# Kernel tuning notes

Measured on AMD Instinct MI355X. Metric: run time of the kernel, lower is better.

## Reference

```python
import jax, jax.numpy as jnp
import numpy as np

L_SPAN = 8          # max event span length
MAX_ITER = 3        # args.max_iteration + 1
RATE = 0.3          # confidence threshold for edge creation
BETA_INTRA = 0.7
BETA_INTER = 0.3


def setup_inputs() -> dict:
    key = jax.random.key(0)
    ks = jax.random.split(key, 16)
    n_sents, S, D = 64, 512, 768
    E, P, NL, H, C = 2000, 20000, 128, 512, 3
    sc = lambda fan: 1.0 / np.sqrt(fan)
    return {
        'sent_emb': jax.random.normal(ks[0], (n_sents, S, D), jnp.float32),
        'W_proj': jax.random.normal(ks[1], (D, NL), jnp.float32) * sc(D),
        'W1': jax.random.normal(ks[2], (2 * D + NL, H), jnp.float32) * sc(2 * D + NL),
        'b1': jnp.zeros((H,), jnp.float32),
        'W2': jax.random.normal(ks[3], (H, C), jnp.float32) * sc(H),
        'b2': jnp.zeros((C,), jnp.float32),
        'W_self': jax.random.normal(ks[4], (NL, NL), jnp.float32) * sc(NL),
        'W_intra': jax.random.normal(ks[5], (NL, NL), jnp.float32) * sc(NL),
        'W_inter': jax.random.normal(ks[6], (NL, NL), jnp.float32) * sc(NL),
        'event_sent': jax.random.randint(ks[7], (E,), 0, n_sents, jnp.int32),
        'event_start': jax.random.randint(ks[8], (E,), 0, S - L_SPAN, jnp.int32),
        'event_len': jax.random.randint(ks[9], (E,), 0, L_SPAN, jnp.int32),
        'pair1': jax.random.randint(ks[10], (P,), 0, E, jnp.int32),
        'pair2': jax.random.randint(ks[11], (P,), 0, E, jnp.int32),
        'rel_type': jax.random.randint(ks[12], (P,), 0, 2, jnp.int32),
        'target': jax.random.randint(ks[13], (P,), 0, 3, jnp.int32),
    }


def _extract_events(sent_emb, event_sent, event_start, event_len):
    # ragged span mean: spans have length 1..L_SPAN
    S = sent_emb.shape[1]
    lens = (event_len + 1).astype(sent_emb.dtype)            # [E]
    offs = jnp.arange(L_SPAN)
    idx = jnp.clip(event_start[:, None] + offs[None, :], 0, S - 1)  # [E, L]
    tok = sent_emb[event_sent[:, None], idx]                 # [E, L, D] gather
    mask = (offs[None, :] < (event_len + 1)[:, None]).astype(sent_emb.dtype)
    return (tok * mask[:, :, None]).sum(1) / lens[:, None]   # [E, D]


def reference(sent_emb, W_proj, W1, b1, W2, b2, W_self, W_intra, W_inter,
              event_sent, event_start, event_len, pair1, pair2, rel_type, target):
    E = event_sent.shape[0]
    e_emb = _extract_events(sent_emb, event_sent, event_start, event_len)   # [E, 768]
    event_pair_embed = jnp.concatenate([e_emb[pair1], e_emb[pair2]], axis=-1)  # [P, 1536]
    x = e_emb @ W_proj                                                      # [E, n_last]

    seg = jax.ops.segment_sum
    loss = jnp.float32(0.0)
    logits = None
    for it in range(MAX_ITER):
        diff = x[pair1] - x[pair2]                                          # [P, n_last]
        feats = jnp.concatenate([event_pair_embed, diff], axis=-1)          # [P, 1536+n_last]
        logits = jax.nn.relu(feats @ W1 + b1) @ W2 + b2                     # [P, C]
        logp = jax.nn.log_softmax(logits, axis=-1)
        ce = -jnp.take_along_axis(logp, target[:, None], axis=-1).mean()
        loss = loss + ce / (it + 1)

        # dynamic graph construction from predictions
        p = jax.nn.softmax(logits, axis=-1)
        conf = p.max(-1) > RATE
        argm = p.argmax(-1)
        f = lambda m: jax.lax.stop_gradient(m.astype(x.dtype))[:, None]
        mi1 = f(conf & (argm == 1) & (rel_type == 0))   # intra: pair1 -> pair2
        mi2 = f(conf & (argm == 2) & (rel_type == 0))   # intra reversed
        me1 = f(conf & (argm == 1) & (rel_type == 1))   # inter
        me2 = f(conf & (argm == 2) & (rel_type == 1))

        # intra aggregation (includes self-loop)
        s_intra = seg(x[pair1] * mi1, pair2, num_segments=E) + \
                  seg(x[pair2] * mi2, pair1, num_segments=E) + x
        c_intra = seg(mi1[:, 0], pair2, num_segments=E) + \
                  seg(mi2[:, 0], pair1, num_segments=E) + 1.0
        agg_intra = s_intra / c_intra[:, None]

        s_inter = seg(x[pair1] * me1, pair2, num_segments=E) + \
                  seg(x[pair2] * me2, pair1, num_segments=E)
        c_inter = seg(me1[:, 0], pair2, num_segments=E) + \
                  seg(me2[:, 0], pair1, num_segments=E)
        agg_inter = s_inter / jnp.maximum(c_inter, 1.0)[:, None]

        x = jax.nn.relu(x @ W_self + BETA_INTRA * (agg_intra @ W_intra)
                        + BETA_INTER * (agg_inter @ W_inter))
    return loss, logits
```

## Files before the change

kernel.cpp:

```cpp
#include <hip/hip_runtime.h>
#include <hip/hip_bf16.h>


#define D_DIM 768
#define H_DIM 512
#define NL_DIM 128

#define FTM 128
#define FTN 64
#define FKB 32
#define FKZ 4

__global__ __launch_bounds__(256) void gemm_fused(
    const float* __restrict__ Ag, const float* __restrict__ W1,
    const float* __restrict__ W_proj,
    float* __restrict__ A1, float* __restrict__ A2, float* __restrict__ X0, int M)
{
    __shared__ float As[2][FKB][FTM + 4];
    __shared__ float Bs[2][FKB][FTN];
    int t = threadIdx.x;
    int bx = blockIdx.x;
    int m0 = blockIdx.y * FTM;
    int kbase = blockIdx.z * (D_DIM / FKZ);
    const float* Bt; float* Ct; int ldb, ldc;
    if (bx < 8)       { Bt = W1 + bx * 64;                           ldb = 512; Ct = A1 + bx * 64;        ldc = 512; }
    else if (bx < 16) { Bt = W1 + (size_t)768 * 512 + (bx - 8) * 64; ldb = 512; Ct = A2 + (bx - 8) * 64;  ldc = 512; }
    else              { Bt = W_proj + (bx - 16) * 64;                ldb = 128; Ct = X0 + (bx - 16) * 64; ldc = 128; }

    int ar  = t >> 3;
    int ac4 = (t & 7) * 4;
    int br  = t >> 4;
    int bc4 = (t & 15) * 4;
    int tm  = t >> 4;
    int tn  = t & 15;

    float acc[8][4] = {};
    const int NT = (D_DIM / FKZ) / FKB;
    float4 pa[4], pb[2];

#pragma unroll
    for (int p = 0; p < 4; ++p) {
        int row = m0 + ar + 32 * p;
        pa[p] = (row < M) ? *(const float4*)(Ag + (size_t)row * D_DIM + kbase + ac4)
                          : make_float4(0.f, 0.f, 0.f, 0.f);
    }
#pragma unroll
    for (int p = 0; p < 2; ++p)
        pb[p] = *(const float4*)(Bt + (size_t)(kbase + br + 16 * p) * ldb + bc4);
#pragma unroll
    for (int p = 0; p < 4; ++p) {
        As[0][ac4 + 0][ar + 32 * p] = pa[p].x;
        As[0][ac4 + 1][ar + 32 * p] = pa[p].y;
        As[0][ac4 + 2][ar + 32 * p] = pa[p].z;
        As[0][ac4 + 3][ar + 32 * p] = pa[p].w;
    }
#pragma unroll
    for (int p = 0; p < 2; ++p)
        *(float4*)&Bs[0][br + 16 * p][bc4] = pb[p];
    __syncthreads();

    for (int kt = 0; kt < NT; ++kt) {
        int b = kt & 1;
        if (kt + 1 < NT) {
            int k0 = kbase + (kt + 1) * FKB;
#pragma unroll
            for (int p = 0; p < 4; ++p) {
                int row = m0 + ar + 32 * p;
                pa[p] = (row < M) ? *(const float4*)(Ag + (size_t)row * D_DIM + k0 + ac4)
                                  : make_float4(0.f, 0.f, 0.f, 0.f);
            }
#pragma unroll
            for (int p = 0; p < 2; ++p)
                pb[p] = *(const float4*)(Bt + (size_t)(k0 + br + 16 * p) * ldb + bc4);
        }
#pragma unroll
        for (int k = 0; k < FKB; ++k) {
            float4 a0 = *(const float4*)&As[b][k][tm * 4];
            float4 a1 = *(const float4*)&As[b][k][64 + tm * 4];
            float4 bv = *(const float4*)&Bs[b][k][tn * 4];
            acc[0][0] += a0.x * bv.x; acc[0][1] += a0.x * bv.y; acc[0][2] += a0.x * bv.z; acc[0][3] += a0.x * bv.w;
            acc[1][0] += a0.y * bv.x; acc[1][1] += a0.y * bv.y; acc[1][2] += a0.y * bv.z; acc[1][3] += a0.y * bv.w;
            acc[2][0] += a0.z * bv.x; acc[2][1] += a0.z * bv.y; acc[2][2] += a0.z * bv.z; acc[2][3] += a0.z * bv.w;
            acc[3][0] += a0.w * bv.x; acc[3][1] += a0.w * bv.y; acc[3][2] += a0.w * bv.z; acc[3][3] += a0.w * bv.w;
            acc[4][0] += a1.x * bv.x; acc[4][1] += a1.x * bv.y; acc[4][2] += a1.x * bv.z; acc[4][3] += a1.x * bv.w;
            acc[5][0] += a1.y * bv.x; acc[5][1] += a1.y * bv.y; acc[5][2] += a1.y * bv.z; acc[5][3] += a1.y * bv.w;
            acc[6][0] += a1.z * bv.x; acc[6][1] += a1.z * bv.y; acc[6][2] += a1.z * bv.z; acc[6][3] += a1.z * bv.w;
            acc[7][0] += a1.w * bv.x; acc[7][1] += a1.w * bv.y; acc[7][2] += a1.w * bv.z; acc[7][3] += a1.w * bv.w;
        }
        if (kt + 1 < NT) {
            int nb = (kt + 1) & 1;
#pragma unroll
            for (int p = 0; p < 4; ++p) {
                As[nb][ac4 + 0][ar + 32 * p] = pa[p].x;
                As[nb][ac4 + 1][ar + 32 * p] = pa[p].y;
                As[nb][ac4 + 2][ar + 32 * p] = pa[p].z;
                As[nb][ac4 + 3][ar + 32 * p] = pa[p].w;
            }
#pragma unroll
            for (int p = 0; p < 2; ++p)
                *(float4*)&Bs[nb][br + 16 * p][bc4] = pb[p];
        }
        __syncthreads();
    }
#pragma unroll
    for (int half = 0; half < 2; ++half) {
#pragma unroll
        for (int i = 0; i < 4; ++i) {
            int row = m0 + half * 64 + tm * 4 + i;
            if (row < M) {
                float* cp = Ct + (size_t)row * ldc + tn * 4;
                atomicAdd(&cp[0], acc[half * 4 + i][0]);
                atomicAdd(&cp[1], acc[half * 4 + i][1]);
                atomicAdd(&cp[2], acc[half * 4 + i][2]);
                atomicAdd(&cp[3], acc[half * 4 + i][3]);
            }
        }
    }
}

#define KB 32
#define TM 64
#define TN 64

struct Smem {
    float As[KB][TM + 4];
    float Bs[KB][TN];
};

__device__ __forceinline__ void tile_gemm(
    const float* __restrict__ A, int lda,
    const float* __restrict__ Bt, int ldb,
    int m0, int M, int K, Smem& sm, float acc[4][4], int t)
{
    int tm = t >> 4, tn = t & 15;
    for (int k0 = 0; k0 < K; k0 += KB) {
#pragma unroll
        for (int r = 0; r < 2; ++r) {
            int row = (t >> 3) + 32 * r;
            int c4 = (t & 7) * 4;
            float4 av = make_float4(0.f, 0.f, 0.f, 0.f);
            if (m0 + row < M)
                av = *(const float4*)(A + (size_t)(m0 + row) * lda + k0 + c4);
            sm.As[c4 + 0][row] = av.x;
            sm.As[c4 + 1][row] = av.y;
            sm.As[c4 + 2][row] = av.z;
            sm.As[c4 + 3][row] = av.w;
        }
#pragma unroll
        for (int r = 0; r < 2; ++r) {
            int row = (t >> 4) + 16 * r;
            int c4 = (t & 15) * 4;
            *(float4*)&sm.Bs[row][c4] =
                *(const float4*)(Bt + (size_t)(k0 + row) * ldb + c4);
        }
        __syncthreads();
#pragma unroll
        for (int k = 0; k < KB; ++k) {
            float4 a = *(const float4*)&sm.As[k][tm * 4];
            float4 b = *(const float4*)&sm.Bs[k][tn * 4];
            acc[0][0] += a.x * b.x; acc[0][1] += a.x * b.y; acc[0][2] += a.x * b.z; acc[0][3] += a.x * b.w;
            acc[1][0] += a.y * b.x; acc[1][1] += a.y * b.y; acc[1][2] += a.y * b.z; acc[1][3] += a.y * b.w;
            acc[2][0] += a.z * b.x; acc[2][1] += a.z * b.y; acc[2][2] += a.z * b.z; acc[2][3] += a.z * b.w;
            acc[3][0] += a.w * b.x; acc[3][1] += a.w * b.y; acc[3][2] += a.w * b.z; acc[3][3] += a.w * b.w;
        }
        __syncthreads();
    }
}

__global__ __launch_bounds__(256) void gemm_y_uv(
    const float* __restrict__ x, const float* __restrict__ W1k,
    const float* __restrict__ A1, const float* __restrict__ A2,
    const float* __restrict__ b1,
    float* __restrict__ U, float* __restrict__ V, int M)
{
    __shared__ Smem sm;
    int t = threadIdx.x;
    int n0 = blockIdx.x * TN;
    int m0 = blockIdx.y * TM;
    float acc[4][4] = {};
    tile_gemm(x, NL_DIM, W1k + n0, H_DIM, m0, M, NL_DIM, sm, acc, t);
    int tm = t >> 4, tn = t & 15;
    float4 b1v = *(const float4*)(b1 + n0 + tn * 4);
#pragma unroll
    for (int i = 0; i < 4; ++i) {
        int row = m0 + tm * 4 + i;
        if (row < M) {
            size_t off = (size_t)row * H_DIM + n0 + tn * 4;
            float4 a1v = *(const float4*)(A1 + off);
            float4 a2v = *(const float4*)(A2 + off);
            float4 u, v;
            u.x = acc[i][0] + a1v.x + b1v.x;  v.x = a2v.x - acc[i][0];
            u.y = acc[i][1] + a1v.y + b1v.y;  v.y = a2v.y - acc[i][1];
            u.z = acc[i][2] + a1v.z + b1v.z;  v.z = a2v.z - acc[i][2];
            u.w = acc[i][3] + a1v.w + b1v.w;  v.w = a2v.w - acc[i][3];
            *(float4*)(U + off) = u;
            *(float4*)(V + off) = v;
        }
    }
}

__global__ __launch_bounds__(256) void gemm_update3(
    const float* __restrict__ x, const float* __restrict__ aggI, const float* __restrict__ aggE,
    const float* __restrict__ Ws, const float* __restrict__ Wi, const float* __restrict__ We,
    float* __restrict__ xn, int M)
{
    __shared__ Smem sm;
    int t = threadIdx.x;
    int n0 = blockIdx.x * TN;
    int m0 = blockIdx.y * TM;
    float acc[4][4] = {};
    tile_gemm(x,    NL_DIM, Ws + n0, NL_DIM, m0, M, NL_DIM, sm, acc, t);
    tile_gemm(aggI, NL_DIM, Wi + n0, NL_DIM, m0, M, NL_DIM, sm, acc, t);
    tile_gemm(aggE, NL_DIM, We + n0, NL_DIM, m0, M, NL_DIM, sm, acc, t);
    int tm = t >> 4, tn = t & 15;
#pragma unroll
    for (int i = 0; i < 4; ++i) {
        int row = m0 + tm * 4 + i;
        if (row < M)
            *(float4*)(xn + (size_t)row * NL_DIM + n0 + tn * 4) =
                make_float4(fmaxf(acc[i][0], 0.f), fmaxf(acc[i][1], 0.f),
                            fmaxf(acc[i][2], 0.f), fmaxf(acc[i][3], 0.f));
    }
}

__global__ __launch_bounds__(192) void extract_kernel(
    const float* __restrict__ sent_emb, const int* __restrict__ es,
    const int* __restrict__ st, const int* __restrict__ el,
    float* __restrict__ e_emb)
{
    int e = blockIdx.x;
    int t = threadIdx.x;
    int s = es[e];
    int start = st[e];
    int len = el[e] + 1;
    const float* base = sent_emb + ((size_t)s * 512 + start) * D_DIM;
    float4 a = make_float4(0.f, 0.f, 0.f, 0.f);
    for (int k = 0; k < len; ++k) {
        float4 v = ((const float4*)(base + (size_t)k * D_DIM))[t];
        a.x += v.x; a.y += v.y; a.z += v.z; a.w += v.w;
    }
    float inv = 1.0f / (float)len;
    ((float4*)(e_emb + (size_t)e * D_DIM))[t] =
        make_float4(a.x * inv, a.y * inv, a.z * inv, a.w * inv);
}

__global__ __launch_bounds__(256) void zero4_kernel(float4* __restrict__ p, int n4)
{
    int i = blockIdx.x * 256 + threadIdx.x;
    if (i < n4) p[i] = make_float4(0.f, 0.f, 0.f, 0.f);
}

__global__ __launch_bounds__(256) void pair_kernel(
    const float* __restrict__ U, const float* __restrict__ V,
    const float* __restrict__ X, const float* __restrict__ W2,
    const float* __restrict__ b2,
    const int* __restrict__ pair1, const int* __restrict__ pair2,
    const int* __restrict__ rel, const int* __restrict__ tgt,
    float* s_intra, float* s_inter, float* c_intra, float* c_inter,
    float* __restrict__ ce_out, float* logits_out, int P, int do_scatter)
{
    __shared__ float ce_sh[4];
    int t = threadIdx.x;
    int wave = t >> 6;
    int lane = t & 63;
    int base = lane * 8;
    float w2f[24];
    {
        const float4* w2p = (const float4*)(W2 + (size_t)base * 3);
#pragma unroll
        for (int q = 0; q < 6; ++q) *(float4*)&w2f[q * 4] = w2p[q];
    }
    float b20 = b2[0], b21 = b2[1], b22 = b2[2];
    int p0 = (blockIdx.x * 4 + wave) * 4;

    int pi1[4], pi2[4];
#pragma unroll
    for (int q = 0; q < 4; ++q) {
        int p = min(p0 + q, P - 1);
        pi1[q] = pair1[p];
        pi2[q] = pair2[p];
    }
    float uf[4][8], vf[4][8];
#pragma unroll
    for (int q = 0; q < 4; ++q) {
        const float4* up = (const float4*)(U + (size_t)pi1[q] * H_DIM + base);
        const float4* vp = (const float4*)(V + (size_t)pi2[q] * H_DIM + base);
        *(float4*)&uf[q][0] = up[0]; *(float4*)&uf[q][4] = up[1];
        *(float4*)&vf[q][0] = vp[0]; *(float4*)&vf[q][4] = vp[1];
    }

    float ce = 0.f;
#pragma unroll
    for (int q = 0; q < 4; ++q) {
        int p = p0 + q;
        if (p >= P) break;
        float l0 = 0.f, l1 = 0.f, l2 = 0.f;
#pragma unroll
        for (int i = 0; i < 8; ++i) {
            float h = fmaxf(uf[q][i] + vf[q][i], 0.f);
            l0 += h * w2f[i * 3 + 0];
            l1 += h * w2f[i * 3 + 1];
            l2 += h * w2f[i * 3 + 2];
        }
#pragma unroll
        for (int off = 32; off > 0; off >>= 1) {
            l0 += __shfl_xor(l0, off);
            l1 += __shfl_xor(l1, off);
            l2 += __shfl_xor(l2, off);
        }
        l0 += b20; l1 += b21; l2 += b22;
        float m = fmaxf(l0, fmaxf(l1, l2));
        float lse = m + logf(expf(l0 - m) + expf(l1 - m) + expf(l2 - m));
        int tg = tgt[p];
        float lt = (tg == 0) ? l0 : ((tg == 1) ? l1 : l2);
        ce += lse - lt;
        if (logits_out && lane == 0) {
            logits_out[(size_t)p * 3 + 0] = l0;
            logits_out[(size_t)p * 3 + 1] = l1;
            logits_out[(size_t)p * 3 + 2] = l2;
        }
        if (do_scatter) {
            int argm = 0; float mx = l0;
            if (l1 > mx) { mx = l1; argm = 1; }
            if (l2 > mx) { mx = l2; argm = 2; }
            if (argm != 0) {
                int r = rel[p];
                int src = (argm == 1) ? pi1[q] : pi2[q];
                int dst = (argm == 1) ? pi2[q] : pi1[q];
                float* sacc = (r == 0) ? s_intra : s_inter;
                float* cacc = (r == 0) ? c_intra : c_inter;
                const float* xs = X + (size_t)src * NL_DIM;
                float* sd = sacc + (size_t)dst * NL_DIM;
                atomicAdd(&sd[lane], xs[lane]);
                atomicAdd(&sd[lane + 64], xs[lane + 64]);
                if (lane == 0) atomicAdd(&cacc[dst], 1.0f);
            }
        }
    }
    if (lane == 0) ce_sh[wave] = ce;
    __syncthreads();
    if (t == 0) ce_out[blockIdx.x] = ce_sh[0] + ce_sh[1] + ce_sh[2] + ce_sh[3];
}

__global__ __launch_bounds__(256) void agg_kernel(
    const float* __restrict__ s_intra, const float* __restrict__ s_inter,
    const float* __restrict__ c_intra, const float* __restrict__ c_inter,
    const float* __restrict__ X,
    float* __restrict__ aggI, float* __restrict__ aggE, int n)
{
    int i = blockIdx.x * 256 + threadIdx.x;
    if (i >= n) return;
    int e = i >> 7;
    float ci = c_intra[e] + 1.0f;
    float cf = fmaxf(c_inter[e], 1.0f);
    aggI[i] = 0.7f * (s_intra[i] + X[i]) / ci;
    aggE[i] = 0.3f * s_inter[i] / cf;
}

__global__ __launch_bounds__(256) void loss_kernel(
    const float* __restrict__ ce, int nblk, int P, float* __restrict__ out)
{
    int t = threadIdx.x;
    float acc = 0.f;
    for (int it = 0; it < 3; ++it) {
        float w = 1.0f / ((float)P * (float)(it + 1));
        for (int i = t; i < nblk; i += 256)
            acc += ce[(size_t)it * nblk + i] * w;
    }
    __shared__ float red[256];
    red[t] = acc;
    __syncthreads();
    for (int s = 128; s > 0; s >>= 1) {
        if (t < s) red[t] += red[t + s];
        __syncthreads();
    }
    if (t == 0) out[0] = red[0];
}

extern "C" void kernel_launch(void* const* d_in, const int* in_sizes, int n_in,
                              void* d_out, int out_size, void* d_ws, size_t ws_size,
                              hipStream_t stream)
{
    const float* sent_emb  = (const float*)d_in[0];
    const float* W_proj    = (const float*)d_in[1];
    const float* W1        = (const float*)d_in[2];
    const float* b1        = (const float*)d_in[3];
    const float* W2        = (const float*)d_in[4];
    const float* b2        = (const float*)d_in[5];
    const float* W_self    = (const float*)d_in[6];
    const float* W_intra   = (const float*)d_in[7];
    const float* W_inter   = (const float*)d_in[8];
    const int* event_sent  = (const int*)d_in[9];
    const int* event_start = (const int*)d_in[10];
    const int* event_len   = (const int*)d_in[11];
    const int* pair1       = (const int*)d_in[12];
    const int* pair2       = (const int*)d_in[13];
    const int* rel_type    = (const int*)d_in[14];
    const int* target      = (const int*)d_in[15];

    int E = in_sizes[9];
    int P = in_sizes[12];
    float* out = (float*)d_out;
    float* ws  = (float*)d_ws;

    size_t o = 0;
    float* e_emb   = ws + o; o += (size_t)E * D_DIM;
    float* A1      = ws + o; o += (size_t)E * H_DIM;
    float* A2      = ws + o; o += (size_t)E * H_DIM;
    float* X0      = ws + o; o += (size_t)E * NL_DIM;
    float* V       = ws + o; o += (size_t)E * H_DIM;
    float* X1      = ws + o; o += (size_t)E * NL_DIM;
    float* s_intra = ws + o; o += (size_t)E * NL_DIM;
    float* s_inter = ws + o; o += (size_t)E * NL_DIM;
    float* c_intra = ws + o; o += (size_t)E;
    float* c_inter = ws + o; o += (size_t)E;
    float* aggI    = ws + o; o += (size_t)E * NL_DIM;
    float* aggE    = ws + o; o += (size_t)E * NL_DIM;
    int NBLK = (P + 15) / 16;
    float* ceb     = ws + o; o += (size_t)3 * NBLK;
    float* U       = e_emb;

    int cz4 = E * (H_DIM * 2 + NL_DIM) / 4;
    zero4_kernel<<<(cz4 + 255) / 256, 256, 0, stream>>>((float4*)A1, cz4);
    extract_kernel<<<E, 192, 0, stream>>>(sent_emb, event_sent, event_start, event_len, e_emb);

    dim3 gF(18, (E + FTM - 1) / FTM, FKZ);
    gemm_fused<<<gF, 256, 0, stream>>>(e_emb, W1, W_proj, A1, A2, X0, E);

    const float* W1k = W1 + (size_t)2 * D_DIM * H_DIM;
    dim3 gY(H_DIM / TN, (E + TM - 1) / TM);
    dim3 gU(NL_DIM / TN, (E + TM - 1) / TM);
    float* xcur = X0;
    float* xnext = X1;
    int zn4 = (E * NL_DIM * 2 + E * 2) / 4;
    for (int it = 0; it < 3; ++it) {
        int last = (it == 2);
        gemm_y_uv<<<gY, 256, 0, stream>>>(xcur, W1k, A1, A2, b1, U, V, E);
        if (!last)
            zero4_kernel<<<(zn4 + 255) / 256, 256, 0, stream>>>((float4*)s_intra, zn4);
        pair_kernel<<<NBLK, 256, 0, stream>>>(U, V, xcur, W2, b2,
                                              pair1, pair2, rel_type, target,
                                              s_intra, s_inter, c_intra, c_inter,
                                              ceb + (size_t)it * NBLK,
                                              last ? (out + 1) : nullptr, P, !last);
        if (!last) {
            agg_kernel<<<(E * NL_DIM + 255) / 256, 256, 0, stream>>>(
                s_intra, s_inter, c_intra, c_inter, xcur, aggI, aggE, E * NL_DIM);
            gemm_update3<<<gU, 256, 0, stream>>>(xcur, aggI, aggE, W_self, W_intra, W_inter, xnext, E);
            float* tmp = xcur; xcur = xnext; xnext = tmp;
        }
    }
    loss_kernel<<<1, 256, 0, stream>>>(ceb, NBLK, P, out);
}
```

Before: 537.0 us.

## Drop split-K atomics in fused GEMM, fold zeroing and aggregation into GEMMs

The big projection GEMM no longer splits K across four blocks with atomic adds. It now uses 64-thread blocks, each computing an 8x8 register tile per thread over the full K range with plain vector stores, which also removes the initial zero-fill of A1/A2/X0. The per-iteration zeroing of the scatter buffers moves into the tail of gemm_y_uv, and the agg_kernel normalisation is folded into the A-tile loads of gemm_update3, removing two launches and the aggI/aggE round trip per iteration. The trade-off is much lower parallelism in the projection GEMM (about 32x18 blocks of 64 threads) and higher register pressure from the 64 accumulators.

Result: slower. 708.1 us (+31.9%).

```diff
diff --git a/kernel.cpp b/kernel.cpp
--- a/kernel.cpp
+++ b/kernel.cpp
@@ -6,114 +6,107 @@
 #define H_DIM 512
 #define NL_DIM 128
 
-#define FTM 128
-#define FTN 64
-#define FKB 32
-#define FKZ 4
-
-__global__ __launch_bounds__(256) void gemm_fused(
+#define GTM 64
+#define GTN 64
+#define GKB 32
+
+__global__ __launch_bounds__(64) void gemm_fused(
     const float* __restrict__ Ag, const float* __restrict__ W1,
     const float* __restrict__ W_proj,
     float* __restrict__ A1, float* __restrict__ A2, float* __restrict__ X0, int M)
 {
-    __shared__ float As[2][FKB][FTM + 4];
-    __shared__ float Bs[2][FKB][FTN];
+    __shared__ float As[2][GKB][GTM + 4];
+    __shared__ float Bs[2][GKB][GTN];
     int t = threadIdx.x;
     int bx = blockIdx.x;
-    int m0 = blockIdx.y * FTM;
-    int kbase = blockIdx.z * (D_DIM / FKZ);
+    int m0 = blockIdx.y * GTM;
     const float* Bt; float* Ct; int ldb, ldc;
     if (bx < 8)       { Bt = W1 + bx * 64;                           ldb = 512; Ct = A1 + bx * 64;        ldc = 512; }
     else if (bx < 16) { Bt = W1 + (size_t)768 * 512 + (bx - 8) * 64; ldb = 512; Ct = A2 + (bx - 8) * 64;  ldc = 512; }
     else              { Bt = W_proj + (bx - 16) * 64;                ldb = 128; Ct = X0 + (bx - 16) * 64; ldc = 128; }
 
-    int ar  = t >> 3;
-    int ac4 = (t & 7) * 4;
-    int br  = t >> 4;
-    int bc4 = (t & 15) * 4;
-    int tm  = t >> 4;
-    int tn  = t & 15;
-
-    float acc[8][4] = {};
-    const int NT = (D_DIM / FKZ) / FKB;
-    float4 pa[4], pb[2];
-
-#pragma unroll
-    for (int p = 0; p < 4; ++p) {
-        int row = m0 + ar + 32 * p;
-        pa[p] = (row < M) ? *(const float4*)(Ag + (size_t)row * D_DIM + kbase + ac4)
-                          : make_float4(0.f, 0.f, 0.f, 0.f);
-    }
-#pragma unroll
-    for (int p = 0; p < 2; ++p)
-        pb[p] = *(const float4*)(Bt + (size_t)(kbase + br + 16 * p) * ldb + bc4);
-#pragma unroll
-    for (int p = 0; p < 4; ++p) {
-        As[0][ac4 + 0][ar + 32 * p] = pa[p].x;
-        As[0][ac4 + 1][ar + 32 * p] = pa[p].y;
-        As[0][ac4 + 2][ar + 32 * p] = pa[p].z;
-        As[0][ac4 + 3][ar + 32 * p] = pa[p].w;
-    }
-#pragma unroll
-    for (int p = 0; p < 2; ++p)
-        *(float4*)&Bs[0][br + 16 * p][bc4] = pb[p];
+    int tm = (t >> 3) * 8;
+    int tn = (t & 7) * 8;
+    bool aval = (m0 + t) < M;
+    const float* arow = Ag + (size_t)(m0 + t) * D_DIM;
+
+    float acc[8][8] = {};
+    float4 pa[8], pb[8];
+    const int NT = D_DIM / GKB;
+
+#pragma unroll
+    for (int j = 0; j < 8; ++j)
+        pa[j] = aval ? *(const float4*)(arow + j * 4) : make_float4(0.f, 0.f, 0.f, 0.f);
+#pragma unroll
+    for (int r = 0; r < 8; ++r) {
+        int idx = t + 64 * r;
+        pb[r] = *(const float4*)(Bt + (size_t)(idx >> 4) * ldb + (idx & 15) * 4);
+    }
+#pragma unroll
+    for (int j = 0; j < 8; ++j) {
+        As[0][4 * j + 0][t] = pa[j].x;
+        As[0][4 * j + 1][t] = pa[j].y;
+        As[0][4 * j + 2][t] = pa[j].z;
+        As[0][4 * j + 3][t] = pa[j].w;
+    }
+#pragma unroll
+    for (int r = 0; r < 8; ++r) {
+        int idx = t + 64 * r;
+        *(float4*)&Bs[0][idx >> 4][(idx & 15) * 4] = pb[r];
+    }
     __syncthreads();
 
     for (int kt = 0; kt < NT; ++kt) {
         int b = kt & 1;
         if (kt + 1 < NT) {
-            int k0 = kbase + (kt + 1) * FKB;
-#pragma unroll
-            for (int p = 0; p < 4; ++p) {
-                int row = m0 + ar + 32 * p;
-                pa[p] = (row < M) ? *(const float4*)(Ag + (size_t)row * D_DIM + k0 + ac4)
-                                  : make_float4(0.f, 0.f, 0.f, 0.f);
+            int k0 = (kt + 1) * GKB;
+#pragma unroll
+            for (int j = 0; j < 8; ++j)
+                pa[j] = aval ? *(const float4*)(arow + k0 + j * 4) : make_float4(0.f, 0.f, 0.f, 0.f);
+#pragma unroll
+            for (int r = 0; r < 8; ++r) {
+                int idx = t + 64 * r;
+                pb[r] = *(const float4*)(Bt + (size_t)(k0 + (idx >> 4)) * ldb + (idx & 15) * 4);
             }
-#pragma unroll
-            for (int p = 0; p < 2; ++p)
-                pb[p] = *(const float4*)(Bt + (size_t)(k0 + br + 16 * p) * ldb + bc4);
-        }
-#pragma unroll
-        for (int k = 0; k < FKB; ++k) {
-            float4 a0 = *(const float4*)&As[b][k][tm * 4];
-            float4 a1 = *(const float4*)&As[b][k][64 + tm * 4];
-            float4 bv = *(const float4*)&Bs[b][k][tn * 4];
-            acc[0][0] += a0.x * bv.x; acc[0][1] += a0.x * bv.y; acc[0][2] += a0.x * bv.z; acc[0][3] += a0.x * bv.w;
-            acc[1][0] += a0.y * bv.x; acc[1][1] += a0.y * bv.y; acc[1][2] += a0.y * bv.z; acc[1][3] += a0.y * bv.w;
-            acc[2][0] += a0.z * bv.x; acc[2][1] += a0.z * bv.y; acc[2][2] += a0.z * bv.z; acc[2][3] += a0.z * bv.w;
-            acc[3][0] += a0.w * bv.x; acc[3][1] += a0.w * bv.y; acc[3][2] += a0.w * bv.z; acc[3][3] += a0.w * bv.w;
-            acc[4][0] += a1.x * bv.x; acc[4][1] += a1.x * bv.y; acc[4][2] += a1.x * bv.z; acc[4][3] += a1.x * bv.w;
-            acc[5][0] += a1.y * bv.x; acc[5][1] += a1.y * bv.y; acc[5][2] += a1.y * bv.z; acc[5][3] += a1.y * bv.w;
-            acc[6][0] += a1.z * bv.x; acc[6][1] += a1.z * bv.y; acc[6][2] += a1.z * bv.z; acc[6][3] += a1.z * bv.w;
-            acc[7][0] += a1.w * bv.x; acc[7][1] += a1.w * bv.y; acc[7][2] += a1.w * bv.z; acc[7][3] += a1.w * bv.w;
+        }
+#pragma unroll
+        for (int k = 0; k < GKB; ++k) {
+            float4 a0 = *(const float4*)&As[b][k][tm];
+            float4 a1 = *(const float4*)&As[b][k][tm + 4];
+            float4 b0 = *(const float4*)&Bs[b][k][tn];
+            float4 b1 = *(const float4*)&Bs[b][k][tn + 4];
+            float av[8] = {a0.x, a0.y, a0.z, a0.w, a1.x, a1.y, a1.z, a1.w};
+            float bv[8] = {b0.x, b0.y, b0.z, b0.w, b1.x, b1.y, b1.z, b1.w};
+#pragma unroll
+            for (int i = 0; i < 8; ++i)
+#pragma unroll
+                for (int j = 0; j < 8; ++j)
+                    acc[i][j] += av[i] * bv[j];
         }
         if (kt + 1 < NT) {
             int nb = (kt + 1) & 1;
 #pragma unroll
-            for (int p = 0; p < 4; ++p) {
-                As[nb][ac4 + 0][ar + 32 * p] = pa[p].x;
-                As[nb][ac4 + 1][ar + 32 * p] = pa[p].y;
-                As[nb][ac4 + 2][ar + 32 * p] = pa[p].z;
-                As[nb][ac4 + 3][ar + 32 * p] = pa[p].w;
+            for (int j = 0; j < 8; ++j) {
+                As[nb][4 * j + 0][t] = pa[j].x;
+                As[nb][4 * j + 1][t] = pa[j].y;
+                As[nb][4 * j + 2][t] = pa[j].z;
+                As[nb][4 * j + 3][t] = pa[j].w;
             }
 #pragma unroll
-            for (int p = 0; p < 2; ++p)
-                *(float4*)&Bs[nb][br + 16 * p][bc4] = pb[p];
+            for (int r = 0; r < 8; ++r) {
+                int idx = t + 64 * r;
+                *(float4*)&Bs[nb][idx >> 4][(idx & 15) * 4] = pb[r];
+            }
         }
         __syncthreads();
     }
 #pragma unroll
-    for (int half = 0; half < 2; ++half) {
-#pragma unroll
-        for (int i = 0; i < 4; ++i) {
-            int row = m0 + half * 64 + tm * 4 + i;
-            if (row < M) {
-                float* cp = Ct + (size_t)row * ldc + tn * 4;
-                atomicAdd(&cp[0], acc[half * 4 + i][0]);
-                atomicAdd(&cp[1], acc[half * 4 + i][1]);
-                atomicAdd(&cp[2], acc[half * 4 + i][2]);
-                atomicAdd(&cp[3], acc[half * 4 + i][3]);
-            }
+    for (int i = 0; i < 8; ++i) {
+        int row = m0 + tm + i;
+        if (row < M) {
+            float* cp = Ct + (size_t)row * ldc + tn;
+            *(float4*)cp       = make_float4(acc[i][0], acc[i][1], acc[i][2], acc[i][3]);
+            *(float4*)(cp + 4) = make_float4(acc[i][4], acc[i][5], acc[i][6], acc[i][7]);
         }
     }
 }
@@ -127,43 +120,27 @@
     float Bs[KB][TN];
 };
 
-__device__ __forceinline__ void tile_gemm(
-    const float* __restrict__ A, int lda,
-    const float* __restrict__ Bt, int ldb,
-    int m0, int M, int K, Smem& sm, float acc[4][4], int t)
-{
-    int tm = t >> 4, tn = t & 15;
-    for (int k0 = 0; k0 < K; k0 += KB) {
-#pragma unroll
-        for (int r = 0; r < 2; ++r) {
-            int row = (t >> 3) + 32 * r;
-            int c4 = (t & 7) * 4;
-            float4 av = make_float4(0.f, 0.f, 0.f, 0.f);
-            if (m0 + row < M)
-                av = *(const float4*)(A + (size_t)(m0 + row) * lda + k0 + c4);
-            sm.As[c4 + 0][row] = av.x;
-            sm.As[c4 + 1][row] = av.y;
-            sm.As[c4 + 2][row] = av.z;
-            sm.As[c4 + 3][row] = av.w;
-        }
-#pragma unroll
-        for (int r = 0; r < 2; ++r) {
-            int row = (t >> 4) + 16 * r;
-            int c4 = (t & 15) * 4;
-            *(float4*)&sm.Bs[row][c4] =
-                *(const float4*)(Bt + (size_t)(k0 + row) * ldb + c4);
-        }
-        __syncthreads();
-#pragma unroll
-        for (int k = 0; k < KB; ++k) {
-            float4 a = *(const float4*)&sm.As[k][tm * 4];
-            float4 b = *(const float4*)&sm.Bs[k][tn * 4];
-            acc[0][0] += a.x * b.x; acc[0][1] += a.x * b.y; acc[0][2] += a.x * b.z; acc[0][3] += a.x * b.w;
-            acc[1][0] += a.y * b.x; acc[1][1] += a.y * b.y; acc[1][2] += a.y * b.z; acc[1][3] += a.y * b.w;
-            acc[2][0] += a.z * b.x; acc[2][1] += a.z * b.y; acc[2][2] += a.z * b.z; acc[2][3] += a.z * b.w;
-            acc[3][0] += a.w * b.x; acc[3][1] += a.w * b.y; acc[3][2] += a.w * b.z; acc[3][3] += a.w * b.w;
-        }
-        __syncthreads();
+__device__ __forceinline__ void tile_compute(Smem& sm, float acc[4][4], int tm, int tn)
+{
+#pragma unroll
+    for (int k = 0; k < KB; ++k) {
+        float4 a = *(const float4*)&sm.As[k][tm * 4];
+        float4 b = *(const float4*)&sm.Bs[k][tn * 4];
+        acc[0][0] += a.x * b.x; acc[0][1] += a.x * b.y; acc[0][2] += a.x * b.z; acc[0][3] += a.x * b.w;
+        acc[1][0] += a.y * b.x; acc[1][1] += a.y * b.y; acc[1][2] += a.y * b.z; acc[1][3] += a.y * b.w;
+        acc[2][0] += a.z * b.x; acc[2][1] += a.z * b.y; acc[2][2] += a.z * b.z; acc[2][3] += a.z * b.w;
+        acc[3][0] += a.w * b.x; acc[3][1] += a.w * b.y; acc[3][2] += a.w * b.z; acc[3][3] += a.w * b.w;
+    }
+}
+
+__device__ __forceinline__ void stage_b(Smem& sm, const float* __restrict__ Bt,
+                                        int k0, int ldb, int t)
+{
+#pragma unroll
+    for (int r = 0; r < 2; ++r) {
+        int row = (t >> 4) + 16 * r;
+        int c4 = (t & 15) * 4;
+        *(float4*)&sm.Bs[row][c4] = *(const float4*)(Bt + (size_t)(k0 + row) * ldb + c4);
     }
 }
 
@@ -171,15 +148,33 @@
     const float* __restrict__ x, const float* __restrict__ W1k,
     const float* __restrict__ A1, const float* __restrict__ A2,
     const float* __restrict__ b1,
-    float* __restrict__ U, float* __restrict__ V, int M)
+    float* __restrict__ U, float* __restrict__ V,
+    float4* __restrict__ zbase, int zn4, int M)
 {
     __shared__ Smem sm;
     int t = threadIdx.x;
     int n0 = blockIdx.x * TN;
     int m0 = blockIdx.y * TM;
+    int tm = t >> 4, tn = t & 15;
+    int ar = t >> 3, c4 = (t & 7) * 4;
     float acc[4][4] = {};
-    tile_gemm(x, NL_DIM, W1k + n0, H_DIM, m0, M, NL_DIM, sm, acc, t);
-    int tm = t >> 4, tn = t & 15;
+    for (int k0 = 0; k0 < NL_DIM; k0 += KB) {
+#pragma unroll
+        for (int r = 0; r < 2; ++r) {
+            int row = m0 + ar + 32 * r;
+            float4 av = make_float4(0.f, 0.f, 0.f, 0.f);
+            if (row < M)
+                av = *(const float4*)(x + (size_t)row * NL_DIM + k0 + c4);
+            sm.As[c4 + 0][ar + 32 * r] = av.x;
+            sm.As[c4 + 1][ar + 32 * r] = av.y;
+            sm.As[c4 + 2][ar + 32 * r] = av.z;
+            sm.As[c4 + 3][ar + 32 * r] = av.w;
+        }
+        stage_b(sm, W1k + n0, k0, H_DIM, t);
+        __syncthreads();
+        tile_compute(sm, acc, tm, tn);
+        __syncthreads();
+    }
     float4 b1v = *(const float4*)(b1 + n0 + tn * 4);
 #pragma unroll
     for (int i = 0; i < 4; ++i) {
@@ -197,10 +192,19 @@
             *(float4*)(V + off) = v;
         }
     }
+    int nb = gridDim.x * gridDim.y;
+    int bid = blockIdx.y * gridDim.x + blockIdx.x;
+    int chunk = (zn4 + nb - 1) / nb;
+    for (int i = t; i < chunk; i += 256) {
+        int idx = bid * chunk + i;
+        if (idx < zn4) zbase[idx] = make_float4(0.f, 0.f, 0.f, 0.f);
+    }
 }
 
 __global__ __launch_bounds__(256) void gemm_update3(
-    const float* __restrict__ x, const float* __restrict__ aggI, const float* __restrict__ aggE,
+    const float* __restrict__ x,
+    const float* __restrict__ s_intra, const float* __restrict__ s_inter,
+    const float* __restrict__ c_intra, const float* __restrict__ c_inter,
     const float* __restrict__ Ws, const float* __restrict__ Wi, const float* __restrict__ We,
     float* __restrict__ xn, int M)
 {
@@ -208,11 +212,43 @@
     int t = threadIdx.x;
     int n0 = blockIdx.x * TN;
     int m0 = blockIdx.y * TM;
+    int tm = t >> 4, tn = t & 15;
+    int ar = t >> 3, c4 = (t & 7) * 4;
     float acc[4][4] = {};
-    tile_gemm(x,    NL_DIM, Ws + n0, NL_DIM, m0, M, NL_DIM, sm, acc, t);
-    tile_gemm(aggI, NL_DIM, Wi + n0, NL_DIM, m0, M, NL_DIM, sm, acc, t);
-    tile_gemm(aggE, NL_DIM, We + n0, NL_DIM, m0, M, NL_DIM, sm, acc, t);
-    int tm = t >> 4, tn = t & 15;
+    for (int ph = 0; ph < 3; ++ph) {
+        const float* Bt = (ph == 0 ? Ws : ph == 1 ? Wi : We) + n0;
+        for (int k0 = 0; k0 < NL_DIM; k0 += KB) {
+#pragma unroll
+            for (int r = 0; r < 2; ++r) {
+                int row = m0 + ar + 32 * r;
+                float4 av = make_float4(0.f, 0.f, 0.f, 0.f);
+                if (row < M) {
+                    size_t off = (size_t)row * NL_DIM + k0 + c4;
+                    if (ph == 0) {
+                        av = *(const float4*)(x + off);
+                    } else if (ph == 1) {
+                        float4 s = *(const float4*)(s_intra + off);
+                        float4 xv = *(const float4*)(x + off);
+                        float sc = 0.7f / (c_intra[row] + 1.0f);
+                        av = make_float4((s.x + xv.x) * sc, (s.y + xv.y) * sc,
+                                         (s.z + xv.z) * sc, (s.w + xv.w) * sc);
+                    } else {
+                        float4 s = *(const float4*)(s_inter + off);
+                        float sc = 0.3f / fmaxf(c_inter[row], 1.0f);
+                        av = make_float4(s.x * sc, s.y * sc, s.z * sc, s.w * sc);
+                    }
+                }
+                sm.As[c4 + 0][ar + 32 * r] = av.x;
+                sm.As[c4 + 1][ar + 32 * r] = av.y;
+                sm.As[c4 + 2][ar + 32 * r] = av.z;
+                sm.As[c4 + 3][ar + 32 * r] = av.w;
+            }
+            stage_b(sm, Bt, k0, NL_DIM, t);
+            __syncthreads();
+            tile_compute(sm, acc, tm, tn);
+            __syncthreads();
+        }
+    }
 #pragma unroll
     for (int i = 0; i < 4; ++i) {
         int row = m0 + tm * 4 + i;
@@ -242,12 +278,6 @@
     float inv = 1.0f / (float)len;
     ((float4*)(e_emb + (size_t)e * D_DIM))[t] =
         make_float4(a.x * inv, a.y * inv, a.z * inv, a.w * inv);
-}
-
-__global__ __launch_bounds__(256) void zero4_kernel(float4* __restrict__ p, int n4)
-{
-    int i = blockIdx.x * 256 + threadIdx.x;
-    if (i < n4) p[i] = make_float4(0.f, 0.f, 0.f, 0.f);
 }
 
 __global__ __launch_bounds__(256) void pair_kernel(
@@ -342,21 +372,6 @@
     if (t == 0) ce_out[blockIdx.x] = ce_sh[0] + ce_sh[1] + ce_sh[2] + ce_sh[3];
 }
 
-__global__ __launch_bounds__(256) void agg_kernel(
-    const float* __restrict__ s_intra, const float* __restrict__ s_inter,
-    const float* __restrict__ c_intra, const float* __restrict__ c_inter,
-    const float* __restrict__ X,
-    float* __restrict__ aggI, float* __restrict__ aggE, int n)
-{
-    int i = blockIdx.x * 256 + threadIdx.x;
-    if (i >= n) return;
-    int e = i >> 7;
-    float ci = c_intra[e] + 1.0f;
-    float cf = fmaxf(c_inter[e], 1.0f);
-    aggI[i] = 0.7f * (s_intra[i] + X[i]) / ci;
-    aggE[i] = 0.3f * s_inter[i] / cf;
-}
-
 __global__ __launch_bounds__(256) void loss_kernel(
     const float* __restrict__ ce, int nblk, int P, float* __restrict__ out)
 {
@@ -414,18 +429,14 @@
     float* s_inter = ws + o; o += (size_t)E * NL_DIM;
     float* c_intra = ws + o; o += (size_t)E;
     float* c_inter = ws + o; o += (size_t)E;
-    float* aggI    = ws + o; o += (size_t)E * NL_DIM;
-    float* aggE    = ws + o; o += (size_t)E * NL_DIM;
     int NBLK = (P + 15) / 16;
     float* ceb     = ws + o; o += (size_t)3 * NBLK;
     float* U       = e_emb;
 
-    int cz4 = E * (H_DIM * 2 + NL_DIM) / 4;
-    zero4_kernel<<<(cz4 + 255) / 256, 256, 0, stream>>>((float4*)A1, cz4);
     extract_kernel<<<E, 192, 0, stream>>>(sent_emb, event_sent, event_start, event_len, e_emb);
 
-    dim3 gF(18, (E + FTM - 1) / FTM, FKZ);
-    gemm_fused<<<gF, 256, 0, stream>>>(e_emb, W1, W_proj, A1, A2, X0, E);
+    dim3 gF(18, (E + GTM - 1) / GTM);
+    gemm_fused<<<gF, 64, 0, stream>>>(e_emb, W1, W_proj, A1, A2, X0, E);
 
     const float* W1k = W1 + (size_t)2 * D_DIM * H_DIM;
     dim3 gY(H_DIM / TN, (E + TM - 1) / TM);
@@ -435,18 +446,16 @@
     int zn4 = (E * NL_DIM * 2 + E * 2) / 4;
     for (int it = 0; it < 3; ++it) {
         int last = (it == 2);
-        gemm_y_uv<<<gY, 256, 0, stream>>>(xcur, W1k, A1, A2, b1, U, V, E);
-        if (!last)
-            zero4_kernel<<<(zn4 + 255) / 256, 256, 0, stream>>>((float4*)s_intra, zn4);
+        gemm_y_uv<<<gY, 256, 0, stream>>>(xcur, W1k, A1, A2, b1, U, V,
+                                          (float4*)s_intra, zn4, E);
         pair_kernel<<<NBLK, 256, 0, stream>>>(U, V, xcur, W2, b2,
                                               pair1, pair2, rel_type, target,
                                               s_intra, s_inter, c_intra, c_inter,
                                               ceb + (size_t)it * NBLK,
                                               last ? (out + 1) : nullptr, P, !last);
         if (!last) {
-            agg_kernel<<<(E * NL_DIM + 255) / 256, 256, 0, stream>>>(
-                s_intra, s_inter, c_intra, c_inter, xcur, aggI, aggE, E * NL_DIM);
-            gemm_update3<<<gU, 256, 0, stream>>>(xcur, aggI, aggE, W_self, W_intra, W_inter, xnext, E);
+            gemm_update3<<<gU, 256, 0, stream>>>(xcur, s_intra, s_inter, c_intra, c_inter,
+                                                 W_self, W_intra, W_inter, xnext, E);
             float* tmp = xcur; xcur = xnext; xnext = tmp;
         }
     }
```
